# Kernel tuning notes

Hardware: AMD Instinct MI355X
Metric: run time of the kernel (lower is better)

Reference implementation:

```python
import jax, jax.numpy as jnp
import numpy as np

B, N, CIN = 8, 4096, 64
S, K, C = 1024, 32, 128      # npoint, k, out_channels
J, DEPTH, H = 5, 2, 4
BETA, EPS = 0.05, 1e-5


def _fps(xyz, npoint):
    # farthest point sampling, deterministic start at index 0
    Bb, Nn = xyz.shape[0], xyz.shape[1]
    bidx = jnp.arange(Bb)

    def step(carry, _):
        dist, far = carry
        cen = xyz[bidx, far][:, None, :]              # [B,1,3]
        d = jnp.sum((xyz - cen) ** 2, -1)             # [B,N]
        dist = jnp.minimum(dist, d)
        nxt = jnp.argmax(dist, axis=1).astype(jnp.int32)
        return (dist, nxt), far

    init = (jnp.full((Bb, Nn), 1e10, xyz.dtype), jnp.zeros((Bb,), jnp.int32))
    _, idxs = jax.lax.scan(step, init, None, length=npoint)
    return idxs.T                                      # [B,npoint]


def _ln(x, g, b):
    mu = jnp.mean(x, -1, keepdims=True)
    v = jnp.mean((x - mu) ** 2, -1, keepdims=True)
    return (x - mu) * jax.lax.rsqrt(v + EPS) * g + b


def _forward(xyz, points, w1, g1, b1, w2, g2, b2, w3, g3, b3,
             ws, wb, alpha, wqkv, wo, ln1g, ln1b, ln2g, ln2b):
    gather = jax.vmap(lambda a, i: a[i])
    fps_idx = _fps(xyz, S)
    new_xyz = gather(xyz, fps_idx)                     # [B,S,3]
    # kNN: squared distances from centroids to all points
    d2 = (jnp.sum(new_xyz ** 2, -1)[:, :, None] + jnp.sum(xyz ** 2, -1)[:, None, :]
          - 2.0 * jnp.einsum('bsd,bnd->bsn', new_xyz, xyz))   # [B,S,N]
    idx = jax.lax.top_k(-d2, K)[1]                     # [B,S,K]
    flat = idx.reshape(B, S * K)
    gxyz = gather(xyz, flat).reshape(B, S, K, 3)
    gnorm = gxyz - new_xyz[:, :, None, :]              # relative coords
    gpts = gather(points, flat).reshape(B, S, K, CIN)
    h = jnp.concatenate([gnorm, gpts], -1)             # [B,S,K,67]
    # pointwise shared MLP (1x1 conv + BN(batch stats) + ReLU)
    for w, g, b in ((w1, g1, b1), (w2, g2, b2), (w3, g3, b3)):
        h = jnp.einsum('bskc,oc->bsko', h, w)
        m = jnp.mean(h, (0, 1, 2))
        v = jnp.var(h, (0, 1, 2))
        h = jax.nn.relu((h - m) * jax.lax.rsqrt(v + EPS) * g + b)
    P = B * S
    pf = h.reshape(P, K, C)
    px = gnorm.reshape(P, K, 3)
    # per-patch graph: Gaussian affinity, sigma = mean pairwise distance
    dd = jnp.sum((px[:, :, None] - px[:, None, :]) ** 2, -1)   # [P,K,K]
    sigma = jnp.mean(jnp.sqrt(dd + 1e-12), (1, 2))[:, None, None]
    A = jnp.exp(-dd / (2.0 * sigma ** 2 + 1e-12))
    dinv = jax.lax.rsqrt(jnp.sum(A, -1) + 1e-12)
    I = jnp.eye(K, dtype=pf.dtype)
    L = I - dinv[:, :, None] * A * dinv[:, None, :]
    # heat-kernel wavelets psi_j = exp(-s_j L), 4th-order Taylor
    psis = []
    for j in range(J):
        M = (-BETA * (2.0 ** j)) * L
        T = I + M
        acc = M
        for m in range(2, 5):
            acc = jnp.einsum('pkl,plm->pkm', acc, M) / m
            T = T + acc
        psis.append(T)
    hcur = pf
    for d in range(DEPTH):
        mix = jnp.zeros_like(hcur)
        for j in range(J):
            mix = mix + alpha[d, j] * jnp.einsum('pkl,plc,cd->pkd', psis[j], hcur, ws[d, j])
        hcur = _ln(hcur + jax.nn.relu(mix + wb[d]), ln1g[d], ln1b[d])
        qkv = (hcur @ wqkv[d]).reshape(P, K, 3, H, C // H)
        q, k_, v = qkv[:, :, 0], qkv[:, :, 1], qkv[:, :, 2]      # [P,K,H,dh]
        att = jax.nn.softmax(jnp.einsum('pkhd,plhd->phkl', q, k_) / np.sqrt(C // H).astype(np.float32), axis=-1)
        o = jnp.einsum('phkl,plhd->pkhd', att, v).reshape(P, K, C) @ wo[d]
        hcur = _ln(hcur + o, ln2g[d], ln2b[d])
    out = jnp.max(hcur.reshape(B, S, K, C), axis=2)    # max-pool over k
    return new_xyz, out


def setup_inputs() -> dict:
    key = jax.random.key(0)
    ks = jax.random.split(key, 10)
    nrm = lambda k, shp, sc: jax.random.normal(k, shp, jnp.float32) * sc
    cin = CIN + 3
    return {
        'xyz': jax.random.normal(ks[0], (B, N, 3), jnp.float32),
        'points': jax.random.normal(ks[1], (B, N, CIN), jnp.float32),
        'w1': nrm(ks[2], (64, cin), cin ** -0.5),
        'g1': jnp.ones((64,)), 'b1': jnp.zeros((64,)),
        'w2': nrm(ks[3], (64, 64), 64 ** -0.5),
        'g2': jnp.ones((64,)), 'b2': jnp.zeros((64,)),
        'w3': nrm(ks[4], (C, 64), 64 ** -0.5),
        'g3': jnp.ones((C,)), 'b3': jnp.zeros((C,)),
        'ws': nrm(ks[5], (DEPTH, J, C, C), C ** -0.5),
        'wb': jnp.zeros((DEPTH, C)),
        'alpha': jnp.ones((DEPTH, J)) / J,
        'wqkv': nrm(ks[6], (DEPTH, C, 3 * C), C ** -0.5),
        'wo': nrm(ks[7], (DEPTH, C, C), C ** -0.5),
        'ln1g': jnp.ones((DEPTH, C)), 'ln1b': jnp.zeros((DEPTH, C)),
        'ln2g': jnp.ones((DEPTH, C)), 'ln2b': jnp.zeros((DEPTH, C)),
    }


def reference(xyz, points, w1, g1, b1, w2, g2, b2, w3, g3, b3,
              ws, wb, alpha, wqkv, wo, ln1g, ln1b, ln2g, ln2b):
    return _forward(xyz, points, w1, g1, b1, w2, g2, b2, w3, g3, b3,
                    ws, wb, alpha, wqkv, wo, ln1g, ln1b, ln2g, ln2b)
```

## Files before the change

### kernel.cpp

```cpp
#include <hip/hip_runtime.h>
#include <math.h>

#define NB 8
#define NP 4096
#define NCIN 64
#define NS 1024
#define NK 32
#define NC 128
#define NJ 5
#define NDEPTH 2
#define NH 4
#define NPTS (NB*NS)
#define NM (NPTS*NK)
#define EPSF 1e-5f

typedef float f32x4 __attribute__((ext_vector_type(4)));
typedef short bf16x8 __attribute__((ext_vector_type(8)));
typedef unsigned short ushort_t;
typedef unsigned long long u64;

#define MFMA(a,b,c) __builtin_amdgcn_mfma_f32_16x16x32_bf16(a,b,c,0,0,0)

__device__ __forceinline__ ushort_t f2b(float f) {
  unsigned int u = __float_as_uint(f);
  u = (u + 0x7fffu + ((u >> 16) & 1u)) >> 16;
  return (ushort_t)u;
}
__device__ __forceinline__ float b2f(ushort_t h) {
  unsigned int u = ((unsigned int)h) << 16;
  return __uint_as_float(u);
}

#define DPPMAX(CTRL) { \
  unsigned lo2 = (unsigned)__builtin_amdgcn_update_dpp(0, (int)(unsigned)best, CTRL, 0xf, 0xf, true); \
  unsigned hi2 = (unsigned)__builtin_amdgcn_update_dpp(0, (int)(unsigned)(best >> 32), CTRL, 0xf, 0xf, true); \
  u64 o = ((u64)hi2 << 32) | lo2; \
  if (o > best) best = o; }

__global__ __launch_bounds__(256) void k_fps(const float* __restrict__ xyz,
                                             float* __restrict__ newxyz) {
  const int b = blockIdx.x;
  const int t = threadIdx.x;
  const int lane = t & 63;
  const int w = t >> 6;
  __shared__ float Xl[NP*3];
  __shared__ float cenL[NS*3];
  __shared__ u64 slot[2][4];
  const float* X = xyz + (size_t)b * NP * 3;
  for (int i = t; i < NP*3; i += 256) Xl[i] = X[i];
  __syncthreads();
  float px[16], py[16], pz[16], dist[16];
  unsigned inv[16];
#pragma unroll
  for (int i = 0; i < 16; ++i) {
    int n = t + 256*i;
    px[i] = Xl[3*n]; py[i] = Xl[3*n+1]; pz[i] = Xl[3*n+2];
    dist[i] = 1e10f;
    inv[i] = ~(unsigned)n;
  }
  int far = 0;
  for (int s = 0; s < NS; ++s) {
    float cx = Xl[3*far], cy = Xl[3*far+1], cz = Xl[3*far+2];
    if (t == 0) { cenL[3*s] = cx; cenL[3*s+1] = cy; cenL[3*s+2] = cz; }
    u64 pk[16];
#pragma unroll
    for (int i = 0; i < 16; ++i) {
      float dx = px[i]-cx, dy = py[i]-cy, dz = pz[i]-cz;
      float d = fmaf(dx,dx, fmaf(dy,dy, dz*dz));
      float nd = fminf(dist[i], d);
      dist[i] = nd;
      pk[i] = ((u64)__float_as_uint(nd) << 32) | inv[i];
    }
#pragma unroll
    for (int st = 1; st < 16; st <<= 1)
#pragma unroll
      for (int i = 0; i < 16; i += 2*st)
        pk[i] = pk[i+st] > pk[i] ? pk[i+st] : pk[i];
    u64 best = pk[0];
    DPPMAX(0x111)
    DPPMAX(0x112)
    DPPMAX(0x114)
    DPPMAX(0x118)
    DPPMAX(0x142)
    DPPMAX(0x143)
    if (lane == 63) slot[s&1][w] = best;
    __syncthreads();
    const u64* sl = slot[s&1];
    u64 s0 = sl[0], s1 = sl[1], s2 = sl[2], s3 = sl[3];
    s0 = s1 > s0 ? s1 : s0;
    s2 = s3 > s2 ? s3 : s2;
    s0 = s2 > s0 ? s2 : s0;
    far = (int)(~(unsigned)s0);
  }
  __syncthreads();
  float* o = newxyz + (size_t)b * NS * 3;
  for (int i = t; i < NS*3; i += 256) o[i] = cenL[i];
}

__global__ __launch_bounds__(64) void k_knn(const float* __restrict__ xyz,
                                            const float* __restrict__ newxyz,
                                            int* __restrict__ knn_idx,
                                            float* __restrict__ gnorm) {
  const int p = blockIdx.x;
  const int b = p >> 10;
  const int lane = threadIdx.x;
  const float* X = xyz + (size_t)b * NP * 3;
  __shared__ float d2[NP];
  float cx = newxyz[3*p], cy = newxyz[3*p+1], cz = newxyz[3*p+2];
  float sc = cx*cx + cy*cy + cz*cz;
#pragma unroll 4
  for (int i = 0; i < NP/64; ++i) {
    int n = lane + 64*i;
    float x = X[3*n], y = X[3*n+1], z = X[3*n+2];
    float sx = x*x + y*y + z*z;
    float dot = cx*x + cy*y + cz*z;
    d2[n] = sc + sx - 2.0f*dot;
  }
  for (int it = 0; it < NK; ++it) {
    float bv = 3.0e38f; int bi = 0x7fffffff;
#pragma unroll 8
    for (int i = 0; i < NP/64; ++i) {
      int n = lane + 64*i;
      float v = d2[n];
      if (v < bv) { bv = v; bi = n; }
    }
#pragma unroll
    for (int off = 32; off; off >>= 1) {
      float ov = __shfl_xor(bv, off);
      int   oi = __shfl_xor(bi, off);
      if (ov < bv || (ov == bv && oi < bi)) { bv = ov; bi = oi; }
    }
    if (lane == 0) {
      d2[bi] = 3.3e38f;
      knn_idx[p*NK + it] = bi;
      float* g = gnorm + ((size_t)p*NK + it)*3;
      g[0] = X[3*bi]   - cx;
      g[1] = X[3*bi+1] - cy;
      g[2] = X[3*bi+2] - cz;
    }
  }
}

__global__ __launch_bounds__(256) void k_layer1(const float* __restrict__ points,
                                                const int* __restrict__ knn_idx,
                                                const float* __restrict__ gnorm,
                                                const float* __restrict__ w1,
                                                float* __restrict__ y,
                                                float* __restrict__ stats) {
  const int r0 = blockIdx.x * 64;
  const int t = threadIdx.x;
  __shared__ float Xs[64][69];
  __shared__ float Ws[64][69];
  __shared__ int nid[64];
  __shared__ float ps[4][64], pss[4][64];
  if (t < 64) nid[t] = knn_idx[r0 + t];
  __syncthreads();
  for (int idx = t; idx < 64*67; idx += 256) {
    int r = idx / 67, c = idx % 67;
    int row = r0 + r;
    float v;
    if (c < 3) v = gnorm[(size_t)row*3 + c];
    else {
      int bb = row >> 15;
      int n = nid[r];
      v = points[((size_t)bb*NP + n)*NCIN + (c-3)];
    }
    Xs[r][c] = v;
  }
  for (int idx = t; idx < 64*67; idx += 256) {
    int o = idx / 67, c = idx % 67;
    Ws[o][c] = w1[idx];
  }
  __syncthreads();
  const int col = t & 63;
  const int rb  = t >> 6;
  float s1 = 0.f, s2 = 0.f;
  for (int i = 0; i < 16; ++i) {
    int r = rb + 4*i;
    float acc = 0.f;
#pragma unroll
    for (int c = 0; c < 67; ++c) acc += Xs[r][c] * Ws[col][c];
    y[(size_t)(r0 + r)*64 + col] = acc;
    s1 += acc; s2 += acc*acc;
  }
  ps[rb][col] = s1; pss[rb][col] = s2;
  __syncthreads();
  if (t < 64) {
    float a = ps[0][t]+ps[1][t]+ps[2][t]+ps[3][t];
    float q = pss[0][t]+pss[1][t]+pss[2][t]+pss[3][t];
    atomicAdd(&stats[t], a);
    atomicAdd(&stats[64 + t], q);
  }
}

template <int COUT>
__global__ __launch_bounds__(256) void k_layer(const float* __restrict__ xin,
                                               const float* __restrict__ aff,
                                               const float* __restrict__ w,
                                               float* __restrict__ y,
                                               float* __restrict__ stats) {
  const int r0 = blockIdx.x * 64;
  const int t = threadIdx.x;
  __shared__ float Xs[64][65];
  __shared__ float Ws[COUT][65];
  __shared__ float sa[64], sb[64];
  constexpr int NTR = 256 / COUT;
  __shared__ float ps[NTR][COUT], pss[NTR][COUT];
  if (t < 64) { sa[t] = aff[t]; sb[t] = aff[64 + t]; }
  __syncthreads();
  for (int idx = t; idx < 64*64; idx += 256) {
    int r = idx >> 6, c = idx & 63;
    float v = xin[(size_t)r0*64 + idx];
    Xs[r][c] = fmaxf(sa[c]*v + sb[c], 0.0f);
  }
  for (int idx = t; idx < COUT*64; idx += 256) {
    int o = idx >> 6, c = idx & 63;
    Ws[o][c] = w[idx];
  }
  __syncthreads();
  const int col = t & (COUT-1);
  const int rb  = t / COUT;
  float s1 = 0.f, s2 = 0.f;
  for (int i = 0; i < 64/NTR; ++i) {
    int r = rb + NTR*i;
    float acc = 0.f;
#pragma unroll
    for (int c = 0; c < 64; ++c) acc += Xs[r][c] * Ws[col][c];
    y[(size_t)(r0 + r)*COUT + col] = acc;
    s1 += acc; s2 += acc*acc;
  }
  ps[rb][col] = s1; pss[rb][col] = s2;
  __syncthreads();
  if (t < COUT) {
    float a = 0.f, q = 0.f;
    for (int n = 0; n < NTR; ++n) { a += ps[n][t]; q += pss[n][t]; }
    atomicAdd(&stats[t], a);
    atomicAdd(&stats[COUT + t], q);
  }
}

__global__ void k_finalize(const float* __restrict__ stats, const float* __restrict__ g,
                           const float* __restrict__ b, float* __restrict__ aff, int cout) {
  int t = threadIdx.x;
  if (t < cout) {
    const float inv = 1.0f / (float)NM;
    float m = stats[t] * inv;
    float var = stats[cout + t] * inv - m*m;
    float a = g[t] * rsqrtf(var + EPSF);
    aff[t] = a;
    aff[cout + t] = b[t] - m * a;
  }
}

__global__ __launch_bounds__(256) void k_pack(const float* __restrict__ ws,
                                              const float* __restrict__ wqkv,
                                              const float* __restrict__ wo,
                                              ushort_t* __restrict__ wpk) {
  int gid = blockIdx.x*256 + threadIdx.x;
  const float* src; int N_; int rem;
  if (gid < 163840)      { int mat = gid >> 14; rem = gid & 16383; src = ws  + (size_t)mat*16384; N_ = 128; }
  else if (gid < 262144) { int g2 = gid - 163840; int d = g2/49152; rem = g2 - d*49152; src = wqkv + (size_t)d*49152; N_ = 384; }
  else                   { int g3 = gid - 262144; int d = g3 >> 14; rem = g3 & 16383;  src = wo  + (size_t)d*16384; N_ = 128; }
  int NTN = N_ >> 4;
  int tile = rem >> 9, r = rem & 511;
  int tk = tile / NTN, tn = tile % NTN;
  int lane2 = r >> 3, jj = r & 7;
  int k = tk*32 + (lane2 >> 4)*8 + jj;
  int n = tn*16 + (lane2 & 15);
  wpk[gid] = f2b(src[(size_t)k*N_ + n]);
}

__global__ __launch_bounds__(256) void k_group(
    const float* __restrict__ h3, const float* __restrict__ aff3,
    const float* __restrict__ gnorm,
    const ushort_t* __restrict__ wpk,
    const float* __restrict__ wb, const float* __restrict__ alpha,
    const float* __restrict__ ln1g, const float* __restrict__ ln1b,
    const float* __restrict__ ln2g, const float* __restrict__ ln2b,
    float* __restrict__ out) {
  const int p = blockIdx.x;
  const int t = threadIdx.x;
  const int lane = t & 63;
  const int w = t >> 6;

  __shared__ __align__(16) float    hcurS[NK*NC];
  __shared__ __align__(16) ushort_t hbS[NK*NC];
  __shared__ __align__(16) ushort_t psisS[5*32*40];
  __shared__ __align__(16) unsigned char scratch[44160];

  float*    ddAF = (float*)scratch;
  float*    pxF  = (float*)(scratch + 4224);
  float*    dinvF= (float*)(scratch + 4608);
  float*    sigF = (float*)(scratch + 4736);
  ushort_t* LbS  = (ushort_t*)(scratch + 4768);
  ushort_t* PmS  = (ushort_t*)(scratch + 7328);
  ushort_t* HjS  = (ushort_t*)scratch;
  float*    uF   = (float*)scratch;
  ushort_t* qS   = (ushort_t*)scratch;
  ushort_t* kS2  = (ushort_t*)(scratch + 8704);
  ushort_t* vTS  = (ushort_t*)(scratch + 17408);
  float*    scoF = (float*)(scratch + 27648);

  if (t < 96) pxF[t] = gnorm[(size_t)p*96 + t];
  const float* h3p = h3 + (size_t)p*4096;
#pragma unroll
  for (int i = 0; i < 16; ++i) {
    int idx = t + 256*i;
    int c = idx & 127, row = idx >> 7;
    float v = fmaxf(aff3[c]*h3p[idx] + aff3[128+c], 0.f);
    hcurS[idx] = v;
    int ha = ((row << 8) + (c << 1)) ^ ((row & 7) << 4);
    hbS[ha >> 1] = f2b(v);
  }
  __syncthreads();
  for (int i = t; i < 1024; i += 256) {
    int k = i >> 5, l = i & 31;
    float dx = pxF[k*3]  -pxF[l*3];
    float dy = pxF[k*3+1]-pxF[l*3+1];
    float dz = pxF[k*3+2]-pxF[l*3+2];
    ddAF[k*33+l] = dx*dx + dy*dy + dz*dz;
  }
  __syncthreads();
  float part = 0.f;
  for (int i = t; i < 1024; i += 256) part += sqrtf(ddAF[(i>>5)*33 + (i&31)] + 1e-12f);
#pragma unroll
  for (int off = 32; off; off >>= 1) part += __shfl_xor(part, off);
  if (lane == 0) sigF[w] = part;
  __syncthreads();
  if (t == 0) {
    float sg = (sigF[0]+sigF[1]+sigF[2]+sigF[3]) * (1.0f/1024.0f);
    sigF[4] = 2.0f*sg*sg + 1e-12f;
  }
  __syncthreads();
  const float denom = sigF[4];
  for (int i = t; i < 1024; i += 256) {
    int k = i >> 5, l = i & 31;
    ddAF[k*33+l] = expf(-ddAF[k*33+l] / denom);
  }
  __syncthreads();
  if (t < 32) {
    float s = 0.f;
    for (int l = 0; l < 32; ++l) s += ddAF[t*33 + l];
    dinvF[t] = rsqrtf(s + 1e-12f);
  }
  __syncthreads();
  for (int i = t; i < 1024; i += 256) {
    int k = i >> 5, l = i & 31;
    float v = -(dinvF[k] * ddAF[k*33+l] * dinvF[l]);
    if (k == l) v += 1.0f;
    LbS[k*40+l] = f2b(v);
  }
  __syncthreads();
  {
    int mi = w >> 1, ni = w & 1;
    int arow = (mi*16 + (lane & 15))*80 + ((lane >> 4) << 4);
    int brow = (ni*16 + (lane & 15))*80 + ((lane >> 4) << 4);
    bf16x8 bfr = *(const bf16x8*)((const char*)LbS + brow);
#pragma unroll
    for (int m = 2; m <= 4; ++m) {
      const ushort_t* Asrc = (m == 2) ? LbS : (PmS + (m-3)*1280);
      bf16x8 afr = *(const bf16x8*)((const char*)Asrc + arow);
      f32x4 z = {0.f,0.f,0.f,0.f};
      f32x4 pv = MFMA(afr, bfr, z);
      int rb2 = mi*16 + (lane >> 4)*4;
      int cl = ni*16 + (lane & 15);
#pragma unroll
      for (int r = 0; r < 4; ++r) PmS[(m-2)*1280 + (rb2+r)*40 + cl] = f2b(pv[r]);
      __syncthreads();
    }
  }
  for (int i = t; i < 1024; i += 256) {
    int k = i >> 5, l = i & 31;
    float lb = b2f(LbS[k*40+l]);
    float p2 = b2f(PmS[k*40+l]);
    float p3 = b2f(PmS[1280 + k*40+l]);
    float p4 = b2f(PmS[2560 + k*40+l]);
    float diag = (k == l) ? 1.0f : 0.0f;
#pragma unroll
    for (int j = 0; j < NJ; ++j) {
      float sj = -0.05f * (float)(1 << j);
      float c2 = 0.5f*sj*sj;
      float c3 = c2*sj*(1.0f/3.0f);
      float c4 = c3*sj*0.25f;
      psisS[j*1280 + k*40 + l] = f2b(diag + sj*lb + c2*p2 + c3*p3 + c4*p4);
    }
  }
  __syncthreads();

  for (int d = 0; d < NDEPTH; ++d) {
    f32x4 m00 = {0.f,0.f,0.f,0.f}, m01 = m00, m10 = m00, m11 = m00;
    for (int j = 0; j < NJ; ++j) {
      __syncthreads();
      const ushort_t* Wp = wpk + (size_t)(d*NJ + j)*16384;
      const float alj = alpha[d*NJ + j];
#pragma unroll
      for (int tni = 0; tni < 2; ++tni) {
        int tn = 2*w + tni;
        f32x4 acc0 = {0.f,0.f,0.f,0.f}, acc1 = acc0;
#pragma unroll
        for (int tk = 0; tk < 4; ++tk) {
          bf16x8 b = *(const bf16x8*)(Wp + ((tk*8 + tn) << 9) + (lane << 3));
          int row0 = lane & 15;
          int ba0 = ((row0 << 8) + (tk << 6) + ((lane >> 4) << 4)) ^ ((row0 & 7) << 4);
          bf16x8 a0 = *(const bf16x8*)((const char*)hbS + ba0);
          acc0 = MFMA(a0, b, acc0);
          int row1 = 16 + (lane & 15);
          int ba1 = ((row1 << 8) + (tk << 6) + ((lane >> 4) << 4)) ^ ((row1 & 7) << 4);
          bf16x8 a1 = *(const bf16x8*)((const char*)hbS + ba1);
          acc1 = MFMA(a1, b, acc1);
        }
        int c = tn*16 + (lane & 15);
        int rbase = (lane >> 4) * 4;
#pragma unroll
        for (int r = 0; r < 4; ++r) {
          HjS[c*40 + rbase + r]      = f2b(alj * acc0[r]);
          HjS[c*40 + 16 + rbase + r] = f2b(alj * acc1[r]);
        }
      }
      __syncthreads();
      {
        const char* psj = (const char*)(psisS + j*1280);
        int koff = (lane >> 4) << 4;
        bf16x8 pa0 = *(const bf16x8*)(psj + (lane & 15)*80 + koff);
        bf16x8 pa1 = *(const bf16x8*)(psj + (16 + (lane & 15))*80 + koff);
        int n0 = 2*w*16 + (lane & 15);
        bf16x8 hb0 = *(const bf16x8*)((const char*)HjS + n0*80 + koff);
        bf16x8 hb1 = *(const bf16x8*)((const char*)HjS + (n0 + 16)*80 + koff);
        m00 = MFMA(pa0, hb0, m00);
        m01 = MFMA(pa0, hb1, m01);
        m10 = MFMA(pa1, hb0, m10);
        m11 = MFMA(pa1, hb1, m11);
      }
    }
    __syncthreads();
    {
      int c0 = 32*w + (lane & 15);
      int c1 = c0 + 16;
      int r0 = (lane >> 4) * 4;
      float wb0 = wb[d*NC + c0], wb1 = wb[d*NC + c1];
#pragma unroll
      for (int r = 0; r < 4; ++r) {
        int row0 = r0 + r, row1 = 16 + r0 + r;
        uF[row0*NC + c0] = hcurS[row0*NC + c0] + fmaxf(m00[r] + wb0, 0.f);
        uF[row0*NC + c1] = hcurS[row0*NC + c1] + fmaxf(m01[r] + wb1, 0.f);
        uF[row1*NC + c0] = hcurS[row1*NC + c0] + fmaxf(m10[r] + wb0, 0.f);
        uF[row1*NC + c1] = hcurS[row1*NC + c1] + fmaxf(m11[r] + wb1, 0.f);
      }
    }
    __syncthreads();
    {
      const int k = t >> 3, e = t & 7;
      float s = 0.f;
#pragma unroll
      for (int ii = 0; ii < 16; ++ii) s += uF[k*NC + e + 8*ii];
      s += __shfl_xor(s,1); s += __shfl_xor(s,2); s += __shfl_xor(s,4);
      float mu = s * (1.0f/128.0f);
      float vs = 0.f;
#pragma unroll
      for (int ii = 0; ii < 16; ++ii) { float dx = uF[k*NC + e + 8*ii] - mu; vs += dx*dx; }
      vs += __shfl_xor(vs,1); vs += __shfl_xor(vs,2); vs += __shfl_xor(vs,4);
      float rs = rsqrtf(vs*(1.0f/128.0f) + EPSF);
#pragma unroll
      for (int ii = 0; ii < 16; ++ii) {
        int o = e + 8*ii;
        float hv = (uF[k*NC + o] - mu)*rs*ln1g[d*NC + o] + ln1b[d*NC + o];
        hcurS[k*NC + o] = hv;
        int ha = ((k << 8) + (o << 1)) ^ ((k & 7) << 4);
        hbS[ha >> 1] = f2b(hv);
      }
    }
    __syncthreads();
    const ushort_t* Wq = wpk + 163840 + (size_t)d*49152;
#pragma unroll
    for (int ti = 0; ti < 12; ++ti) {
      int tile = w + 4*ti;
      int mi = (tile >= 24) ? 1 : 0;
      int tn = tile - 24*mi;
      int comp = tn >> 3;
      int cb = (tn & 7) * 16;
      f32x4 acc = {0.f,0.f,0.f,0.f};
#pragma unroll
      for (int tk = 0; tk < 4; ++tk) {
        bf16x8 b = *(const bf16x8*)(Wq + ((tk*24 + tn) << 9) + (lane << 3));
        int row = mi*16 + (lane & 15);
        int ba = ((row << 8) + (tk << 6) + ((lane >> 4) << 4)) ^ ((row & 7) << 4);
        bf16x8 a = *(const bf16x8*)((const char*)hbS + ba);
        acc = MFMA(a, b, acc);
      }
      int cl = cb + (lane & 15);
      int rb2 = mi*16 + (lane >> 4)*4;
      if (comp == 0) {
#pragma unroll
        for (int r = 0; r < 4; ++r) qS[(rb2+r)*136 + cl] = f2b(acc[r]);
      } else if (comp == 1) {
#pragma unroll
        for (int r = 0; r < 4; ++r) kS2[(rb2+r)*136 + cl] = f2b(acc[r]);
      } else {
#pragma unroll
        for (int r = 0; r < 4; ++r) vTS[cl*40 + rb2 + r] = f2b(acc[r]);
      }
    }
    __syncthreads();
#pragma unroll
    for (int ti = 0; ti < 4; ++ti) {
      int tile = w + 4*ti;
      int h = tile >> 2, mi = (tile >> 1) & 1, ni = tile & 1;
      int koff = h*64 + ((lane >> 4) << 4);
      bf16x8 qa = *(const bf16x8*)((const char*)qS  + (mi*16 + (lane & 15))*272 + koff);
      bf16x8 kb = *(const bf16x8*)((const char*)kS2 + (ni*16 + (lane & 15))*272 + koff);
      f32x4 z = {0.f,0.f,0.f,0.f};
      f32x4 sc = MFMA(qa, kb, z);
      int colL = h*32 + ni*16 + (lane & 15);
      int rb2 = mi*16 + (lane >> 4)*4;
#pragma unroll
      for (int r = 0; r < 4; ++r) scoF[(rb2 + r)*129 + colL] = sc[r] * 0.17677669529663687f;
    }
    __syncthreads();
    {
      int unit = t >> 1, e = t & 1;
      int row = unit & 31, h = unit >> 5;
      const float* srow = scoF + row*129 + h*32 + e*16;
      float v[16];
      float mx = -3.4e38f;
#pragma unroll
      for (int q = 0; q < 16; ++q) { v[q] = srow[q]; mx = fmaxf(mx, v[q]); }
      mx = fmaxf(mx, __shfl_xor(mx, 1));
      float s = 0.f;
#pragma unroll
      for (int q = 0; q < 16; ++q) { v[q] = expf(v[q] - mx); s += v[q]; }
      s += __shfl_xor(s, 1);
      float inv = 1.0f / s;
      ushort_t* arow = qS + row*136 + h*32 + e*16;
#pragma unroll
      for (int q = 0; q < 16; ++q) arow[q] = f2b(v[q] * inv);
    }
    __syncthreads();
#pragma unroll
    for (int ti = 0; ti < 4; ++ti) {
      int tile = w + 4*ti;
      int h = tile >> 2, mi = (tile >> 1) & 1, ni = tile & 1;
      bf16x8 aa = *(const bf16x8*)((const char*)qS + (mi*16 + (lane & 15))*272 + h*64 + ((lane >> 4) << 4));
      bf16x8 vb = *(const bf16x8*)((const char*)vTS + (h*32 + ni*16 + (lane & 15))*80 + ((lane >> 4) << 4));
      f32x4 z = {0.f,0.f,0.f,0.f};
      f32x4 ov = MFMA(aa, vb, z);
      int col = h*32 + ni*16 + (lane & 15);
      int rb2 = mi*16 + (lane >> 4)*4;
#pragma unroll
      for (int r = 0; r < 4; ++r) {
        int row = rb2 + r;
        int ha = ((row << 8) + (col << 1)) ^ ((row & 7) << 4);
        hbS[ha >> 1] = f2b(ov[r]);
      }
    }
    __syncthreads();
    const ushort_t* Wop = wpk + 262144 + (size_t)d*16384;
#pragma unroll
    for (int tni = 0; tni < 2; ++tni) {
      int tn = 2*w + tni;
      f32x4 acc0 = {0.f,0.f,0.f,0.f}, acc1 = acc0;
#pragma unroll
      for (int tk = 0; tk < 4; ++tk) {
        bf16x8 b = *(const bf16x8*)(Wop + ((tk*8 + tn) << 9) + (lane << 3));
        int row0 = lane & 15;
        int ba0 = ((row0 << 8) + (tk << 6) + ((lane >> 4) << 4)) ^ ((row0 & 7) << 4);
        bf16x8 a0 = *(const bf16x8*)((const char*)hbS + ba0);
        acc0 = MFMA(a0, b, acc0);
        int row1 = 16 + (lane & 15);
        int ba1 = ((row1 << 8) + (tk << 6) + ((lane >> 4) << 4)) ^ ((row1 & 7) << 4);
        bf16x8 a1 = *(const bf16x8*)((const char*)hbS + ba1);
        acc1 = MFMA(a1, b, acc1);
      }
      int c = tn*16 + (lane & 15);
      int rb2 = (lane >> 4)*4;
#pragma unroll
      for (int r = 0; r < 4; ++r) {
        uF[(rb2 + r)*NC + c]      = hcurS[(rb2 + r)*NC + c]      + acc0[r];
        uF[(16 + rb2 + r)*NC + c] = hcurS[(16 + rb2 + r)*NC + c] + acc1[r];
      }
    }
    __syncthreads();
    {
      const int k = t >> 3, e = t & 7;
      float s = 0.f;
#pragma unroll
      for (int ii = 0; ii < 16; ++ii) s += uF[k*NC + e + 8*ii];
      s += __shfl_xor(s,1); s += __shfl_xor(s,2); s += __shfl_xor(s,4);
      float mu = s * (1.0f/128.0f);
      float vs = 0.f;
#pragma unroll
      for (int ii = 0; ii < 16; ++ii) { float dx = uF[k*NC + e + 8*ii] - mu; vs += dx*dx; }
      vs += __shfl_xor(vs,1); vs += __shfl_xor(vs,2); vs += __shfl_xor(vs,4);
      float rs = rsqrtf(vs*(1.0f/128.0f) + EPSF);
#pragma unroll
      for (int ii = 0; ii < 16; ++ii) {
        int o = e + 8*ii;
        float hv = (uF[k*NC + o] - mu)*rs*ln2g[d*NC + o] + ln2b[d*NC + o];
        hcurS[k*NC + o] = hv;
        int ha = ((k << 8) + (o << 1)) ^ ((k & 7) << 4);
        hbS[ha >> 1] = f2b(hv);
      }
    }
    __syncthreads();
  }
  if (t < NC) {
    float m = hcurS[t];
    for (int k = 1; k < NK; ++k) m = fmaxf(m, hcurS[k*NC + t]);
    out[(size_t)p*NC + t] = m;
  }
}

extern "C" void kernel_launch(void* const* d_in, const int* in_sizes, int n_in,
                              void* d_out, int out_size, void* d_ws, size_t ws_size,
                              hipStream_t stream) {
  const float* xyz    = (const float*)d_in[0];
  const float* points = (const float*)d_in[1];
  const float* w1     = (const float*)d_in[2];
  const float* g1     = (const float*)d_in[3];
  const float* b1     = (const float*)d_in[4];
  const float* w2     = (const float*)d_in[5];
  const float* g2     = (const float*)d_in[6];
  const float* b2     = (const float*)d_in[7];
  const float* w3     = (const float*)d_in[8];
  const float* g3     = (const float*)d_in[9];
  const float* b3     = (const float*)d_in[10];
  const float* wsW    = (const float*)d_in[11];
  const float* wb     = (const float*)d_in[12];
  const float* alpha  = (const float*)d_in[13];
  const float* wqkv   = (const float*)d_in[14];
  const float* wo     = (const float*)d_in[15];
  const float* ln1g   = (const float*)d_in[16];
  const float* ln1b   = (const float*)d_in[17];
  const float* ln2g   = (const float*)d_in[18];
  const float* ln2b   = (const float*)d_in[19];
  float* outp = (float*)d_out;

  float* wsf   = (float*)d_ws;
  float* gnorm = wsf;
  float* stats = wsf + 786432;
  float* aff   = wsf + 787200;
  int*   knn   = (int*)(wsf + 787968);
  ushort_t* wpk = (ushort_t*)(wsf + 787968);
  float* h2    = wsf + 1050112;
  float* hX    = wsf + 17827328;

  hipMemsetAsync(stats, 0, 768*sizeof(float), stream);
  k_fps<<<NB, 256, 0, stream>>>(xyz, outp);
  k_knn<<<NPTS, 64, 0, stream>>>(xyz, outp, knn, gnorm);
  k_layer1<<<NM/64, 256, 0, stream>>>(points, knn, gnorm, w1, hX, stats);
  k_pack<<<294912/256, 256, 0, stream>>>(wsW, wqkv, wo, wpk);
  k_finalize<<<1, 128, 0, stream>>>(stats, g1, b1, aff, 64);
  k_layer<64><<<NM/64, 256, 0, stream>>>(hX, aff, w2, h2, stats + 256);
  k_finalize<<<1, 128, 0, stream>>>(stats + 256, g2, b2, aff + 256, 64);
  k_layer<128><<<NM/64, 256, 0, stream>>>(h2, aff + 256, w3, hX, stats + 512);
  k_finalize<<<1, 128, 0, stream>>>(stats + 512, g3, b3, aff + 512, 128);
  k_group<<<NPTS, 256, 0, stream>>>(hX, aff + 512, gnorm, wpk, wb, alpha,
                                    ln1g, ln1b, ln2g, ln2b, outp + (size_t)NB*NS*3);
}
```

Measured before the change: 1.833 ms.

## Keep group-kernel activations in registers, fuse LayerNorm and softmax via DPP, streamline FPS

```diff
diff --git a/kernel.cpp b/kernel.cpp
--- a/kernel.cpp
+++ b/kernel.cpp
@@ -31,6 +31,21 @@
   return __uint_as_float(u);
 }
 
+template<int CTRL>
+__device__ __forceinline__ float dpp_f(float v) {
+  return __int_as_float(__builtin_amdgcn_update_dpp(0, __float_as_int(v), CTRL, 0xf, 0xf, true));
+}
+__device__ __forceinline__ float dpp_sum16(float v) {
+  v += dpp_f<0xB1>(v); v += dpp_f<0x4E>(v);
+  v += dpp_f<0x141>(v); v += dpp_f<0x140>(v);
+  return v;
+}
+__device__ __forceinline__ float dpp_max16(float v) {
+  v = fmaxf(v, dpp_f<0xB1>(v)); v = fmaxf(v, dpp_f<0x4E>(v));
+  v = fmaxf(v, dpp_f<0x141>(v)); v = fmaxf(v, dpp_f<0x140>(v));
+  return v;
+}
+
 #define DPPMAX(CTRL) { \
   unsigned lo2 = (unsigned)__builtin_amdgcn_update_dpp(0, (int)(unsigned)best, CTRL, 0xf, 0xf, true); \
   unsigned hi2 = (unsigned)__builtin_amdgcn_update_dpp(0, (int)(unsigned)(best >> 32), CTRL, 0xf, 0xf, true); \
@@ -45,7 +60,8 @@
   const int w = t >> 6;
   __shared__ float Xl[NP*3];
   __shared__ float cenL[NS*3];
-  __shared__ u64 slot[2][4];
+  __shared__ u64 slotP[2][4];
+  __shared__ __align__(16) float slotC[2][4][4];
   const float* X = xyz + (size_t)b * NP * 3;
   for (int i = t; i < NP*3; i += 256) Xl[i] = X[i];
   __syncthreads();
@@ -58,9 +74,8 @@
     dist[i] = 1e10f;
     inv[i] = ~(unsigned)n;
   }
-  int far = 0;
+  float cx = Xl[0], cy = Xl[1], cz = Xl[2];
   for (int s = 0; s < NS; ++s) {
-    float cx = Xl[3*far], cy = Xl[3*far+1], cz = Xl[3*far+2];
     if (t == 0) { cenL[3*s] = cx; cenL[3*s+1] = cy; cenL[3*s+2] = cz; }
     u64 pk[16];
 #pragma unroll
@@ -83,14 +98,25 @@
     DPPMAX(0x118)
     DPPMAX(0x142)
     DPPMAX(0x143)
-    if (lane == 63) slot[s&1][w] = best;
+    if (lane == 63) {
+      slotP[s&1][w] = best;
+      int bi3 = 3 * (int)(~(unsigned)best);
+      slotC[s&1][w][0] = Xl[bi3];
+      slotC[s&1][w][1] = Xl[bi3+1];
+      slotC[s&1][w][2] = Xl[bi3+2];
+    }
     __syncthreads();
-    const u64* sl = slot[s&1];
-    u64 s0 = sl[0], s1 = sl[1], s2 = sl[2], s3 = sl[3];
-    s0 = s1 > s0 ? s1 : s0;
-    s2 = s3 > s2 ? s3 : s2;
-    s0 = s2 > s0 ? s2 : s0;
-    far = (int)(~(unsigned)s0);
+    const int par = s & 1;
+    u64 s0 = slotP[par][0], s1 = slotP[par][1], s2 = slotP[par][2], s3 = slotP[par][3];
+    f32x4 c0v = *(const f32x4*)&slotC[par][0][0];
+    f32x4 c1v = *(const f32x4*)&slotC[par][1][0];
+    f32x4 c2v = *(const f32x4*)&slotC[par][2][0];
+    f32x4 c3v = *(const f32x4*)&slotC[par][3][0];
+    u64 m = s0; f32x4 cw = c0v;
+    if (s1 > m) { m = s1; cw = c1v; }
+    if (s2 > m) { m = s2; cw = c2v; }
+    if (s3 > m) { m = s3; cw = c3v; }
+    cx = cw[0]; cy = cw[1]; cz = cw[2];
   }
   __syncthreads();
   float* o = newxyz + (size_t)b * NS * 3;
@@ -270,7 +296,7 @@
   wpk[gid] = f2b(src[(size_t)k*N_ + n]);
 }
 
-__global__ __launch_bounds__(256) void k_group(
+__global__ __launch_bounds__(256, 3) void k_group(
     const float* __restrict__ h3, const float* __restrict__ aff3,
     const float* __restrict__ gnorm,
     const ushort_t* __restrict__ wpk,
@@ -282,11 +308,12 @@
   const int t = threadIdx.x;
   const int lane = t & 63;
   const int w = t >> 6;
-
-  __shared__ __align__(16) float    hcurS[NK*NC];
+  const int lo16 = lane & 15;
+  const int hi4 = lane >> 4;
+
   __shared__ __align__(16) ushort_t hbS[NK*NC];
   __shared__ __align__(16) ushort_t psisS[5*32*40];
-  __shared__ __align__(16) unsigned char scratch[44160];
+  __shared__ __align__(16) unsigned char scratch[27648];
 
   float*    ddAF = (float*)scratch;
   float*    pxF  = (float*)(scratch + 4224);
@@ -294,12 +321,12 @@
   float*    sigF = (float*)(scratch + 4736);
   ushort_t* LbS  = (ushort_t*)(scratch + 4768);
   ushort_t* PmS  = (ushort_t*)(scratch + 7328);
-  ushort_t* HjS  = (ushort_t*)scratch;
-  float*    uF   = (float*)scratch;
   ushort_t* qS   = (ushort_t*)scratch;
   ushort_t* kS2  = (ushort_t*)(scratch + 8704);
   ushort_t* vTS  = (ushort_t*)(scratch + 17408);
-  float*    scoF = (float*)(scratch + 27648);
+  float*    rowStat = (float*)(scratch + 20480);
+
+  const int c0 = 32*w + lo16, c1 = c0 + 16;
 
   if (t < 96) pxF[t] = gnorm[(size_t)p*96 + t];
   const float* h3p = h3 + (size_t)p*4096;
@@ -308,9 +335,21 @@
     int idx = t + 256*i;
     int c = idx & 127, row = idx >> 7;
     float v = fmaxf(aff3[c]*h3p[idx] + aff3[128+c], 0.f);
-    hcurS[idx] = v;
     int ha = ((row << 8) + (c << 1)) ^ ((row & 7) << 4);
     hbS[ha >> 1] = f2b(v);
+  }
+  float hc[2][2][4];
+  {
+    float ga0 = aff3[c0], gb0 = aff3[128+c0];
+    float ga1 = aff3[c1], gb1 = aff3[128+c1];
+#pragma unroll
+    for (int mi = 0; mi < 2; ++mi)
+#pragma unroll
+      for (int r = 0; r < 4; ++r) {
+        int row = mi*16 + hi4*4 + r;
+        hc[mi][0][r] = fmaxf(ga0*h3p[row*NC + c0] + gb0, 0.f);
+        hc[mi][1][r] = fmaxf(ga1*h3p[row*NC + c1] + gb1, 0.f);
+      }
   }
   __syncthreads();
   for (int i = t; i < 1024; i += 256) {
@@ -352,9 +391,9 @@
   }
   __syncthreads();
   {
-    int mi = w >> 1, ni = w & 1;
-    int arow = (mi*16 + (lane & 15))*80 + ((lane >> 4) << 4);
-    int brow = (ni*16 + (lane & 15))*80 + ((lane >> 4) << 4);
+    int mi2 = w >> 1, ni2 = w & 1;
+    int arow = (mi2*16 + lo16)*80 + (hi4 << 4);
+    int brow = (ni2*16 + lo16)*80 + (hi4 << 4);
     bf16x8 bfr = *(const bf16x8*)((const char*)LbS + brow);
 #pragma unroll
     for (int m = 2; m <= 4; ++m) {
@@ -362,8 +401,8 @@
       bf16x8 afr = *(const bf16x8*)((const char*)Asrc + arow);
       f32x4 z = {0.f,0.f,0.f,0.f};
       f32x4 pv = MFMA(afr, bfr, z);
-      int rb2 = mi*16 + (lane >> 4)*4;
-      int cl = ni*16 + (lane & 15);
+      int rb2 = mi2*16 + hi4*4;
+      int cl = ni2*16 + lo16;
 #pragma unroll
       for (int r = 0; r < 4; ++r) PmS[(m-2)*1280 + (rb2+r)*40 + cl] = f2b(pv[r]);
       __syncthreads();
@@ -379,95 +418,111 @@
 #pragma unroll
     for (int j = 0; j < NJ; ++j) {
       float sj = -0.05f * (float)(1 << j);
-      float c2 = 0.5f*sj*sj;
-      float c3 = c2*sj*(1.0f/3.0f);
-      float c4 = c3*sj*0.25f;
-      psisS[j*1280 + k*40 + l] = f2b(diag + sj*lb + c2*p2 + c3*p3 + c4*p4);
-    }
-  }
-  __syncthreads();
+      float cc2 = 0.5f*sj*sj;
+      float cc3 = cc2*sj*(1.0f/3.0f);
+      float cc4 = cc3*sj*0.25f;
+      psisS[j*1280 + k*40 + l] = f2b(diag + sj*lb + cc2*p2 + cc3*p3 + cc4*p4);
+    }
+  }
 
   for (int d = 0; d < NDEPTH; ++d) {
     f32x4 m00 = {0.f,0.f,0.f,0.f}, m01 = m00, m10 = m00, m11 = m00;
-    for (int j = 0; j < NJ; ++j) {
+    for (int jp = 0; jp < 3; ++jp) {
+      const int njp = (jp == 2) ? 1 : 2;
       __syncthreads();
-      const ushort_t* Wp = wpk + (size_t)(d*NJ + j)*16384;
-      const float alj = alpha[d*NJ + j];
-#pragma unroll
-      for (int tni = 0; tni < 2; ++tni) {
-        int tn = 2*w + tni;
-        f32x4 acc0 = {0.f,0.f,0.f,0.f}, acc1 = acc0;
-#pragma unroll
-        for (int tk = 0; tk < 4; ++tk) {
-          bf16x8 b = *(const bf16x8*)(Wp + ((tk*8 + tn) << 9) + (lane << 3));
-          int row0 = lane & 15;
-          int ba0 = ((row0 << 8) + (tk << 6) + ((lane >> 4) << 4)) ^ ((row0 & 7) << 4);
-          bf16x8 a0 = *(const bf16x8*)((const char*)hbS + ba0);
-          acc0 = MFMA(a0, b, acc0);
-          int row1 = 16 + (lane & 15);
-          int ba1 = ((row1 << 8) + (tk << 6) + ((lane >> 4) << 4)) ^ ((row1 & 7) << 4);
-          bf16x8 a1 = *(const bf16x8*)((const char*)hbS + ba1);
-          acc1 = MFMA(a1, b, acc1);
+      for (int jj = 0; jj < njp; ++jj) {
+        int j = 2*jp + jj;
+        ushort_t* HjS = (ushort_t*)scratch + jj*5120;
+        const ushort_t* Wp = wpk + (size_t)(d*NJ + j)*16384;
+        const float alj = alpha[d*NJ + j];
+#pragma unroll
+        for (int tni = 0; tni < 2; ++tni) {
+          int tn = 2*w + tni;
+          f32x4 acc0 = {0.f,0.f,0.f,0.f}, acc1 = acc0;
+#pragma unroll
+          for (int tk = 0; tk < 4; ++tk) {
+            bf16x8 bfr = *(const bf16x8*)(Wp + ((tk*8 + tn) << 9) + (lane << 3));
+            int row0 = lo16;
+            int ba0 = ((row0 << 8) + (tk << 6) + (hi4 << 4)) ^ ((row0 & 7) << 4);
+            bf16x8 a0 = *(const bf16x8*)((const char*)hbS + ba0);
+            acc0 = MFMA(a0, bfr, acc0);
+            int row1 = 16 + lo16;
+            int ba1 = ((row1 << 8) + (tk << 6) + (hi4 << 4)) ^ ((row1 & 7) << 4);
+            bf16x8 a1 = *(const bf16x8*)((const char*)hbS + ba1);
+            acc1 = MFMA(a1, bfr, acc1);
+          }
+          int c = tn*16 + lo16;
+          int rbase = hi4*4;
+#pragma unroll
+          for (int r = 0; r < 4; ++r) {
+            HjS[c*40 + rbase + r]      = f2b(alj * acc0[r]);
+            HjS[c*40 + 16 + rbase + r] = f2b(alj * acc1[r]);
+          }
         }
-        int c = tn*16 + (lane & 15);
-        int rbase = (lane >> 4) * 4;
-#pragma unroll
-        for (int r = 0; r < 4; ++r) {
-          HjS[c*40 + rbase + r]      = f2b(alj * acc0[r]);
-          HjS[c*40 + 16 + rbase + r] = f2b(alj * acc1[r]);
-        }
       }
       __syncthreads();
-      {
+      for (int jj = 0; jj < njp; ++jj) {
+        int j = 2*jp + jj;
         const char* psj = (const char*)(psisS + j*1280);
-        int koff = (lane >> 4) << 4;
-        bf16x8 pa0 = *(const bf16x8*)(psj + (lane & 15)*80 + koff);
-        bf16x8 pa1 = *(const bf16x8*)(psj + (16 + (lane & 15))*80 + koff);
-        int n0 = 2*w*16 + (lane & 15);
-        bf16x8 hb0 = *(const bf16x8*)((const char*)HjS + n0*80 + koff);
-        bf16x8 hb1 = *(const bf16x8*)((const char*)HjS + (n0 + 16)*80 + koff);
+        const char* HjB = (const char*)scratch + jj*10240;
+        int koff = hi4 << 4;
+        bf16x8 pa0 = *(const bf16x8*)(psj + lo16*80 + koff);
+        bf16x8 pa1 = *(const bf16x8*)(psj + (16 + lo16)*80 + koff);
+        bf16x8 hb0 = *(const bf16x8*)(HjB + c0*80 + koff);
+        bf16x8 hb1 = *(const bf16x8*)(HjB + c1*80 + koff);
         m00 = MFMA(pa0, hb0, m00);
         m01 = MFMA(pa0, hb1, m01);
         m10 = MFMA(pa1, hb0, m10);
         m11 = MFMA(pa1, hb1, m11);
       }
     }
+    float u[2][2][4];
+    {
+      float wb0 = wb[d*NC + c0], wb1 = wb[d*NC + c1];
+#pragma unroll
+      for (int r = 0; r < 4; ++r) {
+        u[0][0][r] = hc[0][0][r] + fmaxf(m00[r] + wb0, 0.f);
+        u[0][1][r] = hc[0][1][r] + fmaxf(m01[r] + wb1, 0.f);
+        u[1][0][r] = hc[1][0][r] + fmaxf(m10[r] + wb0, 0.f);
+        u[1][1][r] = hc[1][1][r] + fmaxf(m11[r] + wb1, 0.f);
+      }
+#pragma unroll
+      for (int mi = 0; mi < 2; ++mi)
+#pragma unroll
+        for (int r = 0; r < 4; ++r) {
+          float s = u[mi][0][r] + u[mi][1][r];
+          float q = u[mi][0][r]*u[mi][0][r] + u[mi][1][r]*u[mi][1][r];
+          s = dpp_sum16(s);
+          q = dpp_sum16(q);
+          if (lo16 == 0) {
+            int row = mi*16 + hi4*4 + r;
+            rowStat[row*8 + w*2]     = s;
+            rowStat[row*8 + w*2 + 1] = q;
+          }
+        }
+    }
     __syncthreads();
     {
-      int c0 = 32*w + (lane & 15);
-      int c1 = c0 + 16;
-      int r0 = (lane >> 4) * 4;
-      float wb0 = wb[d*NC + c0], wb1 = wb[d*NC + c1];
-#pragma unroll
-      for (int r = 0; r < 4; ++r) {
-        int row0 = r0 + r, row1 = 16 + r0 + r;
-        uF[row0*NC + c0] = hcurS[row0*NC + c0] + fmaxf(m00[r] + wb0, 0.f);
-        uF[row0*NC + c1] = hcurS[row0*NC + c1] + fmaxf(m01[r] + wb1, 0.f);
-        uF[row1*NC + c0] = hcurS[row1*NC + c0] + fmaxf(m10[r] + wb0, 0.f);
-        uF[row1*NC + c1] = hcurS[row1*NC + c1] + fmaxf(m11[r] + wb1, 0.f);
-      }
-    }
-    __syncthreads();
-    {
-      const int k = t >> 3, e = t & 7;
-      float s = 0.f;
-#pragma unroll
-      for (int ii = 0; ii < 16; ++ii) s += uF[k*NC + e + 8*ii];
-      s += __shfl_xor(s,1); s += __shfl_xor(s,2); s += __shfl_xor(s,4);
-      float mu = s * (1.0f/128.0f);
-      float vs = 0.f;
-#pragma unroll
-      for (int ii = 0; ii < 16; ++ii) { float dx = uF[k*NC + e + 8*ii] - mu; vs += dx*dx; }
-      vs += __shfl_xor(vs,1); vs += __shfl_xor(vs,2); vs += __shfl_xor(vs,4);
-      float rs = rsqrtf(vs*(1.0f/128.0f) + EPSF);
-#pragma unroll
-      for (int ii = 0; ii < 16; ++ii) {
-        int o = e + 8*ii;
-        float hv = (uF[k*NC + o] - mu)*rs*ln1g[d*NC + o] + ln1b[d*NC + o];
-        hcurS[k*NC + o] = hv;
-        int ha = ((k << 8) + (o << 1)) ^ ((k & 7) << 4);
-        hbS[ha >> 1] = f2b(hv);
-      }
+      float g0 = ln1g[d*NC + c0], b0 = ln1b[d*NC + c0];
+      float g1 = ln1g[d*NC + c1], b1 = ln1b[d*NC + c1];
+#pragma unroll
+      for (int mi = 0; mi < 2; ++mi)
+#pragma unroll
+        for (int r = 0; r < 4; ++r) {
+          int row = mi*16 + hi4*4 + r;
+          f32x4 a = *(const f32x4*)(rowStat + row*8);
+          f32x4 bq = *(const f32x4*)(rowStat + row*8 + 4);
+          float mu = (a[0]+a[2]+bq[0]+bq[2]) * (1.0f/128.0f);
+          float ex2 = (a[1]+a[3]+bq[1]+bq[3]) * (1.0f/128.0f);
+          float rs = rsqrtf(ex2 - mu*mu + EPSF);
+          float h0 = (u[mi][0][r] - mu)*rs*g0 + b0;
+          float h1 = (u[mi][1][r] - mu)*rs*g1 + b1;
+          hc[mi][0][r] = h0; hc[mi][1][r] = h1;
+          int ha0 = ((row << 8) + (c0 << 1)) ^ ((row & 7) << 4);
+          int ha1 = ((row << 8) + (c1 << 1)) ^ ((row & 7) << 4);
+          hbS[ha0 >> 1] = f2b(h0);
+          hbS[ha1 >> 1] = f2b(h1);
+        }
     }
     __syncthreads();
     const ushort_t* Wq = wpk + 163840 + (size_t)d*49152;
@@ -481,14 +536,14 @@
       f32x4 acc = {0.f,0.f,0.f,0.f};
 #pragma unroll
       for (int tk = 0; tk < 4; ++tk) {
-        bf16x8 b = *(const bf16x8*)(Wq + ((tk*24 + tn) << 9) + (lane << 3));
-        int row = mi*16 + (lane & 15);
-        int ba = ((row << 8) + (tk << 6) + ((lane >> 4) << 4)) ^ ((row & 7) << 4);
+        bf16x8 bfr = *(const bf16x8*)(Wq + ((tk*24 + tn) << 9) + (lane << 3));
+        int row = mi*16 + lo16;
+        int ba = ((row << 8) + (tk << 6) + (hi4 << 4)) ^ ((row & 7) << 4);
         bf16x8 a = *(const bf16x8*)((const char*)hbS + ba);
-        acc = MFMA(a, b, acc);
-      }
-      int cl = cb + (lane & 15);
-      int rb2 = mi*16 + (lane >> 4)*4;
+        acc = MFMA(a, bfr, acc);
+      }
+      int cl = cb + lo16;
+      int rb2 = mi*16 + hi4*4;
       if (comp == 0) {
 #pragma unroll
         for (int r = 0; r < 4; ++r) qS[(rb2+r)*136 + cl] = f2b(acc[r]);
@@ -498,6 +553,40 @@
       } else {
 #pragma unroll
         for (int r = 0; r < 4; ++r) vTS[cl*40 + rb2 + r] = f2b(acc[r]);
+      }
+    }
+    __syncthreads();
+    float scr[2][2][4];
+#pragma unroll
+    for (int ti = 0; ti < 2; ++ti) {
+      int pi = w + 4*ti;
+      int h = pi >> 1, mi = pi & 1;
+      int koff = h*64 + (hi4 << 4);
+      bf16x8 qa = *(const bf16x8*)((const char*)qS + (mi*16 + lo16)*272 + koff);
+#pragma unroll
+      for (int ni = 0; ni < 2; ++ni) {
+        bf16x8 kb = *(const bf16x8*)((const char*)kS2 + (ni*16 + lo16)*272 + koff);
+        f32x4 z = {0.f,0.f,0.f,0.f};
+        f32x4 sv = MFMA(qa, kb, z);
+#pragma unroll
+        for (int r = 0; r < 4; ++r) scr[ti][ni][r] = sv[r] * 0.17677669529663687f;
+      }
+    }
+    __syncthreads();
+#pragma unroll
+    for (int ti = 0; ti < 2; ++ti) {
+      int pi = w + 4*ti;
+      int h = pi >> 1, mi = pi & 1;
+#pragma unroll
+      for (int r = 0; r < 4; ++r) {
+        float s0 = scr[ti][0][r], s1 = scr[ti][1][r];
+        float mx = dpp_max16(fmaxf(s0, s1));
+        float e0 = expf(s0 - mx), e1 = expf(s1 - mx);
+        float sum = dpp_sum16(e0 + e1);
+        float iv = 1.0f / sum;
+        int row = mi*16 + hi4*4 + r;
+        qS[row*136 + h*32 + lo16]      = f2b(e0*iv);
+        qS[row*136 + h*32 + 16 + lo16] = f2b(e1*iv);
       }
     }
     __syncthreads();
@@ -505,46 +594,12 @@
     for (int ti = 0; ti < 4; ++ti) {
       int tile = w + 4*ti;
       int h = tile >> 2, mi = (tile >> 1) & 1, ni = tile & 1;
-      int koff = h*64 + ((lane >> 4) << 4);
-      bf16x8 qa = *(const bf16x8*)((const char*)qS  + (mi*16 + (lane & 15))*272 + koff);
-      bf16x8 kb = *(const bf16x8*)((const char*)kS2 + (ni*16 + (lane & 15))*272 + koff);
-      f32x4 z = {0.f,0.f,0.f,0.f};
-      f32x4 sc = MFMA(qa, kb, z);
-      int colL = h*32 + ni*16 + (lane & 15);
-      int rb2 = mi*16 + (lane >> 4)*4;
-#pragma unroll
-      for (int r = 0; r < 4; ++r) scoF[(rb2 + r)*129 + colL] = sc[r] * 0.17677669529663687f;
-    }
-    __syncthreads();
-    {
-      int unit = t >> 1, e = t & 1;
-      int row = unit & 31, h = unit >> 5;
-      const float* srow = scoF + row*129 + h*32 + e*16;
-      float v[16];
-      float mx = -3.4e38f;
-#pragma unroll
-      for (int q = 0; q < 16; ++q) { v[q] = srow[q]; mx = fmaxf(mx, v[q]); }
-      mx = fmaxf(mx, __shfl_xor(mx, 1));
-      float s = 0.f;
-#pragma unroll
-      for (int q = 0; q < 16; ++q) { v[q] = expf(v[q] - mx); s += v[q]; }
-      s += __shfl_xor(s, 1);
-      float inv = 1.0f / s;
-      ushort_t* arow = qS + row*136 + h*32 + e*16;
-#pragma unroll
-      for (int q = 0; q < 16; ++q) arow[q] = f2b(v[q] * inv);
-    }
-    __syncthreads();
-#pragma unroll
-    for (int ti = 0; ti < 4; ++ti) {
-      int tile = w + 4*ti;
-      int h = tile >> 2, mi = (tile >> 1) & 1, ni = tile & 1;
-      bf16x8 aa = *(const bf16x8*)((const char*)qS + (mi*16 + (lane & 15))*272 + h*64 + ((lane >> 4) << 4));
-      bf16x8 vb = *(const bf16x8*)((const char*)vTS + (h*32 + ni*16 + (lane & 15))*80 + ((lane >> 4) << 4));
+      bf16x8 aa = *(const bf16x8*)((const char*)qS + (mi*16 + lo16)*272 + h*64 + (hi4 << 4));
+      bf16x8 vb = *(const bf16x8*)((const char*)vTS + (h*32 + ni*16 + lo16)*80 + (hi4 << 4));
       f32x4 z = {0.f,0.f,0.f,0.f};
       f32x4 ov = MFMA(aa, vb, z);
-      int col = h*32 + ni*16 + (lane & 15);
-      int rb2 = mi*16 + (lane >> 4)*4;
+      int col = h*32 + ni*16 + lo16;
+      int rb2 = mi*16 + hi4*4;
 #pragma unroll
       for (int r = 0; r < 4; ++r) {
         int row = rb2 + r;
@@ -560,52 +615,72 @@
       f32x4 acc0 = {0.f,0.f,0.f,0.f}, acc1 = acc0;
 #pragma unroll
       for (int tk = 0; tk < 4; ++tk) {
-        bf16x8 b = *(const bf16x8*)(Wop + ((tk*8 + tn) << 9) + (lane << 3));
-        int row0 = lane & 15;
-        int ba0 = ((row0 << 8) + (tk << 6) + ((lane >> 4) << 4)) ^ ((row0 & 7) << 4);
+        bf16x8 bfr = *(const bf16x8*)(Wop + ((tk*8 + tn) << 9) + (lane << 3));
+        int row0 = lo16;
+        int ba0 = ((row0 << 8) + (tk << 6) + (hi4 << 4)) ^ ((row0 & 7) << 4);
         bf16x8 a0 = *(const bf16x8*)((const char*)hbS + ba0);
-        acc0 = MFMA(a0, b, acc0);
-        int row1 = 16 + (lane & 15);
-        int ba1 = ((row1 << 8) + (tk << 6) + ((lane >> 4) << 4)) ^ ((row1 & 7) << 4);
+        acc0 = MFMA(a0, bfr, acc0);
+        int row1 = 16 + lo16;
+        int ba1 = ((row1 << 8) + (tk << 6) + (hi4 << 4)) ^ ((row1 & 7) << 4);
         bf16x8 a1 = *(const bf16x8*)((const char*)hbS + ba1);
-        acc1 = MFMA(a1, b, acc1);
-      }
-      int c = tn*16 + (lane & 15);
-      int rb2 = (lane >> 4)*4;
+        acc1 = MFMA(a1, bfr, acc1);
+      }
 #pragma unroll
       for (int r = 0; r < 4; ++r) {
-        uF[(rb2 + r)*NC + c]      = hcurS[(rb2 + r)*NC + c]      + acc0[r];
-        uF[(16 + rb2 + r)*NC + c] = hcurS[(16 + rb2 + r)*NC + c] + acc1[r];
-      }
-    }
+        u[0][tni][r] = hc[0][tni][r] + acc0[r];
+        u[1][tni][r] = hc[1][tni][r] + acc1[r];
+      }
+    }
+#pragma unroll
+    for (int mi = 0; mi < 2; ++mi)
+#pragma unroll
+      for (int r = 0; r < 4; ++r) {
+        float s = u[mi][0][r] + u[mi][1][r];
+        float q = u[mi][0][r]*u[mi][0][r] + u[mi][1][r]*u[mi][1][r];
+        s = dpp_sum16(s);
+        q = dpp_sum16(q);
+        if (lo16 == 0) {
+          int row = mi*16 + hi4*4 + r;
+          rowStat[row*8 + w*2]     = s;
+          rowStat[row*8 + w*2 + 1] = q;
+        }
+      }
     __syncthreads();
     {
-      const int k = t >> 3, e = t & 7;
-      float s = 0.f;
-#pragma unroll
-      for (int ii = 0; ii < 16; ++ii) s += uF[k*NC + e + 8*ii];
-      s += __shfl_xor(s,1); s += __shfl_xor(s,2); s += __shfl_xor(s,4);
-      float mu = s * (1.0f/128.0f);
-      float vs = 0.f;
-#pragma unroll
-      for (int ii = 0; ii < 16; ++ii) { float dx = uF[k*NC + e + 8*ii] - mu; vs += dx*dx; }
-      vs += __shfl_xor(vs,1); vs += __shfl_xor(vs,2); vs += __shfl_xor(vs,4);
-      float rs = rsqrtf(vs*(1.0f/128.0f) + EPSF);
-#pragma unroll
-      for (int ii = 0; ii < 16; ++ii) {
-        int o = e + 8*ii;
-        float hv = (uF[k*NC + o] - mu)*rs*ln2g[d*NC + o] + ln2b[d*NC + o];
-        hcurS[k*NC + o] = hv;
-        int ha = ((k << 8) + (o << 1)) ^ ((k & 7) << 4);
-        hbS[ha >> 1] = f2b(hv);
-      }
-    }
-    __syncthreads();
-  }
-  if (t < NC) {
-    float m = hcurS[t];
-    for (int k = 1; k < NK; ++k) m = fmaxf(m, hcurS[k*NC + t]);
-    out[(size_t)p*NC + t] = m;
+      float g0 = ln2g[d*NC + c0], b0 = ln2b[d*NC + c0];
+      float g1 = ln2g[d*NC + c1], b1 = ln2b[d*NC + c1];
+#pragma unroll
+      for (int mi = 0; mi < 2; ++mi)
+#pragma unroll
+        for (int r = 0; r < 4; ++r) {
+          int row = mi*16 + hi4*4 + r;
+          f32x4 a = *(const f32x4*)(rowStat + row*8);
+          f32x4 bq = *(const f32x4*)(rowStat + row*8 + 4);
+          float mu = (a[0]+a[2]+bq[0]+bq[2]) * (1.0f/128.0f);
+          float ex2 = (a[1]+a[3]+bq[1]+bq[3]) * (1.0f/128.0f);
+          float rs = rsqrtf(ex2 - mu*mu + EPSF);
+          float h0 = (u[mi][0][r] - mu)*rs*g0 + b0;
+          float h1 = (u[mi][1][r] - mu)*rs*g1 + b1;
+          hc[mi][0][r] = h0; hc[mi][1][r] = h1;
+          int ha0 = ((row << 8) + (c0 << 1)) ^ ((row & 7) << 4);
+          int ha1 = ((row << 8) + (c1 << 1)) ^ ((row & 7) << 4);
+          hbS[ha0 >> 1] = f2b(h0);
+          hbS[ha1 >> 1] = f2b(h1);
+        }
+    }
+  }
+  {
+    float v0 = hc[0][0][0], v1 = hc[0][1][0];
+#pragma unroll
+    for (int r = 1; r < 4; ++r) { v0 = fmaxf(v0, hc[0][0][r]); v1 = fmaxf(v1, hc[0][1][r]); }
+#pragma unroll
+    for (int r = 0; r < 4; ++r) { v0 = fmaxf(v0, hc[1][0][r]); v1 = fmaxf(v1, hc[1][1][r]); }
+    v0 = fmaxf(v0, __shfl_xor(v0, 16)); v0 = fmaxf(v0, __shfl_xor(v0, 32));
+    v1 = fmaxf(v1, __shfl_xor(v1, 16)); v1 = fmaxf(v1, __shfl_xor(v1, 32));
+    if (hi4 == 0) {
+      out[(size_t)p*NC + c0] = v0;
+      out[(size_t)p*NC + c1] = v1;
+    }
   }
 }
 
```

Measured after the change: 2.120 ms. +15.6%, slower.
